# Kernel optimization log

Hardware: AMD Instinct MI355X
Metric: run time of the kernel (lower is better)

The kernel has to match this reference:

```python
import jax, jax.numpy as jnp
import numpy as np
import math

T = 1024
HID = 2880
NH = 64      # attention heads
KV = 8       # key/value heads
HD = 64      # head dim
INTER = 2880
QMULT = NH // KV
SM_SCALE = 1.0 / math.sqrt(HD)
ALPHA = 1.702   # swiglu alpha
LIMIT = 7.0     # swiglu clamp limit
EPS = 1e-5
ROPE_BASE = 150000.0
INIT_CTX = 4096
SCALING = 32.0
NTK_ALPHA = 1.0
NTK_BETA = 32.0


def rmsnorm(x, scale):
    t = x * jax.lax.rsqrt(jnp.mean(x * x, axis=-1, keepdims=True) + EPS)
    return t * scale


def rope_cos_sin(num_tokens):
    # YaRN-style NTK interpolation (scaling_factor > 1 branch)
    freq = ROPE_BASE ** (jnp.arange(0, HD, 2, dtype=jnp.float32) / HD)
    concentration = 0.1 * math.log(SCALING) + 1.0
    d_half = HD / 2
    low = d_half * math.log(INIT_CTX / (NTK_BETA * 2 * math.pi)) / math.log(ROPE_BASE)
    high = d_half * math.log(INIT_CTX / (NTK_ALPHA * 2 * math.pi)) / math.log(ROPE_BASE)
    interpolation = 1.0 / (SCALING * freq)
    extrapolation = 1.0 / freq
    ramp = (jnp.arange(d_half, dtype=jnp.float32) - low) / (high - low)
    mask = 1.0 - jnp.clip(ramp, 0.0, 1.0)
    inv_freq = interpolation * (1.0 - mask) + extrapolation * mask
    t = jnp.arange(num_tokens, dtype=jnp.float32)
    freqs = t[:, None] * inv_freq[None, :]           # [T, HD/2]
    return jnp.cos(freqs) * concentration, jnp.sin(freqs) * concentration


def apply_rope(x, cos, sin):
    # x: [T, heads, HD]; cos/sin: [T, HD/2]
    c = cos[:, None, :]
    s = sin[:, None, :]
    x1, x2 = jnp.split(x, 2, axis=-1)
    return jnp.concatenate([x1 * c - x2 * s, x2 * c + x1 * s], axis=-1)


def setup_inputs() -> dict:
    key = jax.random.key(0)
    ks = jax.random.split(key, 10)
    p = lambda k, shape: jax.random.normal(k, shape, jnp.float32) * 0.02
    qkv_dim = HD * (NH + 2 * KV)
    return {
        "x": jax.random.normal(ks[0], (T, HID), jnp.float32),
        "attn_norm_scale": jnp.ones((HID,), jnp.float32),
        "wqkv": p(ks[1], (qkv_dim, HID)),
        "bqkv": p(ks[2], (qkv_dim,)),
        "wout": p(ks[3], (HID, NH * HD)),
        "bout": p(ks[4], (HID,)),
        "mlp_norm_scale": jnp.ones((HID,), jnp.float32),
        "w1": p(ks[5], (2 * INTER, HID)),
        "b1": p(ks[6], (2 * INTER,)),
        "w2": p(ks[7], (HID, INTER)),
        "b2": p(ks[8], (HID,)),
    }


def reference(x, attn_norm_scale, wqkv, bqkv, wout, bout, mlp_norm_scale, w1, b1, w2, b2):
    # ---- attention sub-block ----
    t = rmsnorm(x, attn_norm_scale)
    qkv = t @ wqkv.T + bqkv                                   # [T, 5120]
    q = qkv[:, : NH * HD].reshape(T, NH, HD)
    k = qkv[:, NH * HD : (NH + KV) * HD].reshape(T, KV, HD)
    v = qkv[:, (NH + KV) * HD :].reshape(T, KV, HD)
    cos, sin = rope_cos_sin(T)
    q = apply_rope(q, cos, sin)
    k = apply_rope(k, cos, sin)
    kf = jnp.repeat(k, QMULT, axis=1)                         # GQA expand -> [T, NH, HD]
    vf = jnp.repeat(v, QMULT, axis=1)
    scores = jnp.einsum('thd,shd->hts', q, kf) * SM_SCALE     # [NH, T, T]
    causal = jnp.tril(jnp.ones((T, T), dtype=bool))
    scores = jnp.where(causal[None, :, :], scores, jnp.float32(-1e30))
    attn = jax.nn.softmax(scores, axis=-1)
    o = jnp.einsum('hts,shd->thd', attn, vf).reshape(T, NH * HD)
    h = x + o @ wout.T + bout                                 # residual
    # ---- SwiGLU MLP sub-block ----
    u = rmsnorm(h, mlp_norm_scale) @ w1.T + b1                # [T, 2*INTER] interleaved
    g = jnp.minimum(u[:, ::2], LIMIT)
    lin = jnp.clip(u[:, 1::2], -LIMIT, LIMIT)
    act = g * jax.nn.sigmoid(ALPHA * g) * (lin + 1.0)         # [T, INTER]
    return h + act @ w2.T + b2
```

## Files before the change

### kernel.cpp

```cpp
#include <hip/hip_runtime.h>

typedef unsigned short ushort_t;
typedef unsigned int uint_t;
typedef __bf16 bf16x8 __attribute__((ext_vector_type(8)));
typedef float floatx4 __attribute__((ext_vector_type(4)));

#define T_TOK 1024
#define HID 2880
#define NH 64
#define KV 8
#define HD 64
#define INTER 2880
#define QKV_DIM 5120
#define O_DIM 4096

typedef __attribute__((address_space(1))) const uint_t glb_u32;
typedef __attribute__((address_space(3))) uint_t lds_u32;

__device__ __forceinline__ float b2f(ushort_t u) {
    uint_t i = ((uint_t)u) << 16;
    return __builtin_bit_cast(float, i);
}
__device__ __forceinline__ ushort_t f2b(float f) {
    uint_t i = __builtin_bit_cast(uint_t, f);
    uint_t r = i + 0x7FFFu + ((i >> 16) & 1u);
    return (ushort_t)(r >> 16);
}
__device__ __forceinline__ uint4 ld16(const void* p) { uint4 v; __builtin_memcpy(&v, p, 16); return v; }
__device__ __forceinline__ void st16(void* p, uint4 v) { __builtin_memcpy(p, &v, 16); }
__device__ __forceinline__ float4 ld16f(const void* p) { float4 v; __builtin_memcpy(&v, p, 16); return v; }
__device__ __forceinline__ bf16x8 ldfrag(const void* p) { bf16x8 v; __builtin_memcpy(&v, p, 16); return v; }
__device__ __forceinline__ void cvt8st(void* lds, float4 a, float4 b) {
    ushort_t o[8] = {f2b(a.x), f2b(a.y), f2b(a.z), f2b(a.w),
                     f2b(b.x), f2b(b.y), f2b(b.z), f2b(b.w)};
    __builtin_memcpy(lds, o, 16);
}

__global__ __launch_bounds__(256) void rmsnorm_f2b(
    const float* __restrict__ x, const float* __restrict__ scale,
    ushort_t* __restrict__ out)
{
    const int row = blockIdx.x;
    const int tid = threadIdx.x;
    const float* xr = x + (size_t)row * HID;
    float ss = 0.f;
    for (int i = tid; i < HID / 4; i += 256) {
        float4 v = ld16f(xr + i * 4);
        ss += v.x * v.x + v.y * v.y + v.z * v.z + v.w * v.w;
    }
    #pragma unroll
    for (int m = 32; m >= 1; m >>= 1) ss += __shfl_xor(ss, m, 64);
    __shared__ float red[4];
    if ((tid & 63) == 0) red[tid >> 6] = ss;
    __syncthreads();
    float rstd = rsqrtf((red[0] + red[1] + red[2] + red[3]) / (float)HID + 1e-5f);
    for (int i = tid; i < HID / 8; i += 256) {
        float4 a = ld16f(xr + i * 8);
        float4 b = ld16f(xr + i * 8 + 4);
        float4 sa = ld16f(scale + i * 8);
        float4 sb = ld16f(scale + i * 8 + 4);
        cvt8st(out + (size_t)row * HID + i * 8,
               make_float4(a.x * rstd * sa.x, a.y * rstd * sa.y, a.z * rstd * sa.z, a.w * rstd * sa.w),
               make_float4(b.x * rstd * sb.x, b.y * rstd * sb.y, b.z * rstd * sb.z, b.w * rstd * sb.w));
    }
}

__global__ __launch_bounds__(256) void gemm_bt(
    const ushort_t* __restrict__ A, const float* __restrict__ B,
    const float* __restrict__ bias, const float* residual,
    void* C, int out_f32, int M, int N, int K)
{
    __shared__ ushort_t As[128 * 64];
    __shared__ ushort_t Bs[64 * 64];
    const int tid = threadIdx.x;
    const int lane = tid & 63, wave = tid >> 6;
    const int l15 = lane & 15, quad = lane >> 4;

    const int nbx = N >> 6;
    int flat = (int)blockIdx.x;
    const int cpx = (int)gridDim.x >> 3;
    flat = (flat & 7) * cpx + (flat >> 3);
    const int m0 = (flat / nbx) * 128;
    const int n0 = (flat % nbx) * 64;

    const int wm = (wave >> 1) * 64, wn = (wave & 1) * 32;

    const int arow = wave * 32 + (lane >> 3);
    const int aslot = (lane & 7) ^ (lane >> 3);
    const ushort_t* Abase = A + (size_t)(m0 + arow) * K + aslot * 8;

    const int brow = tid >> 2;
    const int kb = (tid & 3) * 8;
    const int sa = (tid & 3) ^ (brow & 7);
    const int sb = ((tid & 3) + 4) ^ (brow & 7);
    const float* Bbase = B + (size_t)(n0 + brow) * K;

    floatx4 acc[4][2] = {};
    const int nk = K >> 6;
    for (int kt = 0; kt < nk; ++kt) {
        const int k0 = kt << 6;
        float4 f0 = ld16f(Bbase + k0 + kb);
        float4 f1 = ld16f(Bbase + k0 + kb + 4);
        float4 f2 = ld16f(Bbase + k0 + kb + 32);
        float4 f3 = ld16f(Bbase + k0 + kb + 36);
        #pragma unroll
        for (int q = 0; q < 4; q++) {
            __builtin_amdgcn_global_load_lds(
                (glb_u32*)(Abase + (size_t)(q * 8) * K + k0),
                (lds_u32*)(&As[(wave * 4 + q) * 512]),
                16, 0, 0);
        }
        cvt8st(&Bs[brow * 64 + sa * 8], f0, f1);
        cvt8st(&Bs[brow * 64 + sb * 8], f2, f3);
        __syncthreads();
        #pragma unroll
        for (int c = 0; c < 2; c++) {
            bf16x8 af[4], bfr[2];
            #pragma unroll
            for (int i = 0; i < 4; i++) {
                int r = wm + i * 16 + l15;
                af[i] = ldfrag(&As[r * 64 + (((c * 4 + quad) ^ (r & 7)) * 8)]);
            }
            #pragma unroll
            for (int j = 0; j < 2; j++) {
                int r = wn + j * 16 + l15;
                bfr[j] = ldfrag(&Bs[r * 64 + (((c * 4 + quad) ^ (r & 7)) * 8)]);
            }
            #pragma unroll
            for (int i = 0; i < 4; i++)
                #pragma unroll
                for (int j = 0; j < 2; j++)
                    acc[i][j] = __builtin_amdgcn_mfma_f32_16x16x32_bf16(af[i], bfr[j], acc[i][j], 0, 0, 0);
        }
        __syncthreads();
    }
    #pragma unroll
    for (int i = 0; i < 4; i++) {
        int row = m0 + wm + i * 16 + quad * 4;
        #pragma unroll
        for (int j = 0; j < 2; j++) {
            int col = n0 + wn + j * 16 + l15;
            float bv = bias[col];
            #pragma unroll
            for (int r = 0; r < 4; r++) {
                float v = acc[i][j][r] + bv;
                if (residual) v += residual[(size_t)(row + r) * N + col];
                if (out_f32) ((float*)C)[(size_t)(row + r) * N + col] = v;
                else ((ushort_t*)C)[(size_t)(row + r) * N + col] = f2b(v);
            }
        }
    }
}

__global__ __launch_bounds__(256) void rope_kernel(ushort_t* __restrict__ qkv)
{
    int idx = blockIdx.x * 256 + threadIdx.x;
    int d = idx & 31;
    int rest = idx >> 5;
    int head = rest % (NH + KV);
    int tok = rest / (NH + KV);

    const float TWO_PI = 6.2831853071795864f;
    float fd = (float)d;
    float freq = powf(150000.0f, fd * (1.0f / 32.0f));
    float interpolation = 1.0f / (32.0f * freq);
    float extrapolation = 1.0f / freq;
    float lnb = logf(150000.0f);
    float low  = 32.0f * logf(4096.0f / (32.0f * TWO_PI)) / lnb;
    float high = 32.0f * logf(4096.0f / TWO_PI) / lnb;
    float ramp = (fd - low) / (high - low);
    ramp = fminf(fmaxf(ramp, 0.0f), 1.0f);
    float mask = 1.0f - ramp;
    float inv_freq = interpolation * (1.0f - mask) + extrapolation * mask;
    float conc = 0.1f * logf(32.0f) + 1.0f;
    float ang = (float)tok * inv_freq;
    float s = sinf(ang) * conc;
    float c = cosf(ang) * conc;

    size_t base = (head < NH)
        ? (size_t)tok * QKV_DIM + head * HD
        : (size_t)tok * QKV_DIM + NH * HD + (head - NH) * HD;
    float x1 = b2f(qkv[base + d]);
    float x2 = b2f(qkv[base + 32 + d]);
    qkv[base + d]      = f2b(x1 * c - x2 * s);
    qkv[base + 32 + d] = f2b(x2 * c + x1 * s);
}

__global__ __launch_bounds__(256) void attn_kernel(
    const ushort_t* __restrict__ qkv, ushort_t* __restrict__ o)
{
    const int qt = blockIdx.x;
    const int h  = blockIdx.y;
    const int g  = h >> 3;
    const int tid = threadIdx.x;
    const int lane = tid & 63, wave = tid >> 6;
    const int l15 = lane & 15, quad = lane >> 4;

    __shared__ ushort_t Ks[64 * 72];
    __shared__ ushort_t Vt[64 * 72];
    __shared__ ushort_t Ps[4][16 * 72];

    bf16x8 qf[2];
    const int qrow = qt * 64 + wave * 16 + l15;
    #pragma unroll
    for (int c = 0; c < 2; c++)
        qf[c] = ldfrag(&qkv[(size_t)qrow * QKV_DIM + h * HD + quad * 8 + 32 * c]);

    floatx4 ofrag[4] = {};
    float mrow[4], lrow[4];
    #pragma unroll
    for (int r = 0; r < 4; r++) { mrow[r] = -1e30f; lrow[r] = 0.f; }

    for (int kt = 0; kt <= qt; ++kt) {
        {
            int row = tid >> 2;
            int seg = (tid & 3) * 16;
            size_t sb = (size_t)(kt * 64 + row) * QKV_DIM + NH * HD + g * HD;
            st16(&Ks[row * 72 + seg],     ld16(&qkv[sb + seg]));
            st16(&Ks[row * 72 + seg + 8], ld16(&qkv[sb + seg + 8]));
            uint4 v0 = ld16(&qkv[sb + KV * HD + seg]);
            uint4 v1 = ld16(&qkv[sb + KV * HD + seg + 8]);
            uint_t w0[4] = {v0.x, v0.y, v0.z, v0.w};
            uint_t w1[4] = {v1.x, v1.y, v1.z, v1.w};
            #pragma unroll
            for (int e = 0; e < 8; e++) {
                ushort_t s0 = (e & 1) ? (ushort_t)(w0[e >> 1] >> 16) : (ushort_t)(w0[e >> 1] & 0xffffu);
                ushort_t s1 = (e & 1) ? (ushort_t)(w1[e >> 1] >> 16) : (ushort_t)(w1[e >> 1] & 0xffffu);
                Vt[(seg + e) * 72 + row]     = s0;
                Vt[(seg + 8 + e) * 72 + row] = s1;
            }
        }
        __syncthreads();

        floatx4 sf[4];
        #pragma unroll
        for (int j = 0; j < 4; j++) {
            floatx4 z = {};
            #pragma unroll
            for (int c = 0; c < 2; c++) {
                bf16x8 kf = ldfrag(&Ks[(j * 16 + l15) * 72 + quad * 8 + 32 * c]);
                z = __builtin_amdgcn_mfma_f32_16x16x32_bf16(qf[c], kf, z, 0, 0, 0);
            }
            sf[j] = z;
        }
        const int qg = qt * 64 + wave * 16 + quad * 4;
        const int kgb = kt * 64 + l15;
        float rowmax[4];
        #pragma unroll
        for (int r = 0; r < 4; r++) rowmax[r] = -1e30f;
        #pragma unroll
        for (int j = 0; j < 4; j++)
            #pragma unroll
            for (int r = 0; r < 4; r++) {
                float v = sf[j][r] * 0.125f;
                if (kgb + j * 16 > qg + r) v = -1e30f;
                sf[j][r] = v;
                rowmax[r] = fmaxf(rowmax[r], v);
            }
        #pragma unroll
        for (int r = 0; r < 4; r++)
            #pragma unroll
            for (int m = 1; m < 16; m <<= 1)
                rowmax[r] = fmaxf(rowmax[r], __shfl_xor(rowmax[r], m, 64));
        float alpha[4], rowsum[4];
        #pragma unroll
        for (int r = 0; r < 4; r++) {
            float mnew = fmaxf(mrow[r], rowmax[r]);
            alpha[r] = __expf(mrow[r] - mnew);
            mrow[r] = mnew;
            rowsum[r] = 0.f;
        }
        #pragma unroll
        for (int j = 0; j < 4; j++)
            #pragma unroll
            for (int r = 0; r < 4; r++) {
                float p = __expf(sf[j][r] - mrow[r]);
                rowsum[r] += p;
                Ps[wave][(quad * 4 + r) * 72 + j * 16 + l15] = f2b(p);
            }
        #pragma unroll
        for (int r = 0; r < 4; r++) {
            #pragma unroll
            for (int m = 1; m < 16; m <<= 1)
                rowsum[r] += __shfl_xor(rowsum[r], m, 64);
            lrow[r] = lrow[r] * alpha[r] + rowsum[r];
        }
        #pragma unroll
        for (int j = 0; j < 4; j++)
            #pragma unroll
            for (int r = 0; r < 4; r++)
                ofrag[j][r] *= alpha[r];
        __syncthreads();
        #pragma unroll
        for (int c = 0; c < 2; c++) {
            bf16x8 pf = ldfrag(&Ps[wave][l15 * 72 + quad * 8 + 32 * c]);
            #pragma unroll
            for (int j = 0; j < 4; j++) {
                bf16x8 vf = ldfrag(&Vt[(j * 16 + l15) * 72 + quad * 8 + 32 * c]);
                ofrag[j] = __builtin_amdgcn_mfma_f32_16x16x32_bf16(pf, vf, ofrag[j], 0, 0, 0);
            }
        }
        __syncthreads();
    }
    #pragma unroll
    for (int j = 0; j < 4; j++)
        #pragma unroll
        for (int r = 0; r < 4; r++) {
            int row = qt * 64 + wave * 16 + quad * 4 + r;
            int col = h * HD + j * 16 + l15;
            o[(size_t)row * O_DIM + col] = f2b(ofrag[j][r] / lrow[r]);
        }
}

__global__ __launch_bounds__(256) void act_kernel(
    const ushort_t* __restrict__ u, ushort_t* __restrict__ act)
{
    int i = blockIdx.x * 256 + threadIdx.x;
    if (i >= T_TOK * INTER) return;
    int row = i / INTER, c = i % INTER;
    uint_t v; __builtin_memcpy(&v, u + (size_t)row * (2 * INTER) + 2 * c, 4);
    float gt  = b2f((ushort_t)(v & 0xffffu));
    float lin = b2f((ushort_t)(v >> 16));
    gt = fminf(gt, 7.0f);
    lin = fminf(fmaxf(lin, -7.0f), 7.0f);
    float sg = 1.0f / (1.0f + __expf(-1.702f * gt));
    act[i] = f2b(gt * sg * (lin + 1.0f));
}

extern "C" void kernel_launch(void* const* d_in, const int* in_sizes, int n_in,
                              void* d_out, int out_size, void* d_ws, size_t ws_size,
                              hipStream_t stream)
{
    const float* x               = (const float*)d_in[0];
    const float* attn_norm_scale = (const float*)d_in[1];
    const float* wqkv            = (const float*)d_in[2];
    const float* bqkv            = (const float*)d_in[3];
    const float* wout            = (const float*)d_in[4];
    const float* bout            = (const float*)d_in[5];
    const float* mlp_norm_scale  = (const float*)d_in[6];
    const float* w1              = (const float*)d_in[7];
    const float* b1              = (const float*)d_in[8];
    const float* w2              = (const float*)d_in[9];
    const float* b2              = (const float*)d_in[10];
    float* out = (float*)d_out;

    char* ws = (char*)d_ws;
    ushort_t* t   = (ushort_t*)ws;
    ushort_t* qkv = (ushort_t*)(ws + (size_t)T_TOK * HID * 2);
    ushort_t* ob  = (ushort_t*)(ws + (size_t)T_TOK * (HID + QKV_DIM) * 2);
    ushort_t* u   = (ushort_t*)(ws + (size_t)T_TOK * (HID + QKV_DIM + O_DIM) * 2);
    ushort_t* ac  = (ushort_t*)(ws + (size_t)T_TOK * (HID + QKV_DIM + O_DIM + 2 * INTER) * 2);

    rmsnorm_f2b<<<T_TOK, 256, 0, stream>>>(x, attn_norm_scale, t);
    gemm_bt<<<dim3((T_TOK / 128) * (QKV_DIM / 64)), 256, 0, stream>>>(
        t, wqkv, bqkv, nullptr, qkv, 0, T_TOK, QKV_DIM, HID);
    rope_kernel<<<(T_TOK * (NH + KV) * 32) / 256, 256, 0, stream>>>(qkv);
    attn_kernel<<<dim3(T_TOK / 64, NH), 256, 0, stream>>>(qkv, ob);
    gemm_bt<<<dim3((T_TOK / 128) * (HID / 64)), 256, 0, stream>>>(
        ob, wout, bout, x, out, 1, T_TOK, HID, O_DIM);
    rmsnorm_f2b<<<T_TOK, 256, 0, stream>>>(out, mlp_norm_scale, t);
    gemm_bt<<<dim3((T_TOK / 128) * ((2 * INTER) / 64)), 256, 0, stream>>>(
        t, w1, b1, nullptr, u, 0, T_TOK, 2 * INTER, HID);
    act_kernel<<<(T_TOK * INTER + 255) / 256, 256, 0, stream>>>(u, ac);
    gemm_bt<<<dim3((T_TOK / 128) * (HID / 64)), 256, 0, stream>>>(
        ac, w2, b2, out, out, 1, T_TOK, HID, INTER);
}
```

Baseline: 625.5 us.

## Double-buffer GEMM tiles, split-K the output projections, constant-fold RoPE

```diff
diff --git a/kernel.cpp b/kernel.cpp
--- a/kernel.cpp
+++ b/kernel.cpp
@@ -68,10 +68,11 @@
 __global__ __launch_bounds__(256) void gemm_bt(
     const ushort_t* __restrict__ A, const float* __restrict__ B,
     const float* __restrict__ bias, const float* residual,
-    void* C, int out_f32, int M, int N, int K)
-{
-    __shared__ ushort_t As[128 * 64];
-    __shared__ ushort_t Bs[64 * 64];
+    void* C, int out_f32, float* __restrict__ scratch,
+    int M, int N, int K)
+{
+    __shared__ ushort_t As[2][128 * 64];
+    __shared__ ushort_t Bs[2][64 * 64];
     const int tid = threadIdx.x;
     const int lane = tid & 63, wave = tid >> 6;
     const int l15 = lane & 15, quad = lane >> 4;
@@ -85,46 +86,68 @@
 
     const int wm = (wave >> 1) * 64, wn = (wave & 1) * 32;
 
+    const int z = (int)blockIdx.y;
+    const int nk_all = K >> 6;
+    const int nk0 = (nk_all + 1) >> 1;
+    const int kbeg = (gridDim.y > 1 && z) ? (nk0 << 6) : 0;
+    const int nk = (gridDim.y > 1) ? (z ? nk_all - nk0 : nk0) : nk_all;
+
     const int arow = wave * 32 + (lane >> 3);
     const int aslot = (lane & 7) ^ (lane >> 3);
-    const ushort_t* Abase = A + (size_t)(m0 + arow) * K + aslot * 8;
+    const ushort_t* Abase = A + (size_t)(m0 + arow) * K + kbeg + aslot * 8;
 
     const int brow = tid >> 2;
     const int kb = (tid & 3) * 8;
     const int sa = (tid & 3) ^ (brow & 7);
     const int sb = ((tid & 3) + 4) ^ (brow & 7);
-    const float* Bbase = B + (size_t)(n0 + brow) * K;
+    const float* Bbase = B + (size_t)(n0 + brow) * K + kbeg;
 
     floatx4 acc[4][2] = {};
-    const int nk = K >> 6;
+
+    {
+        float4 f0 = ld16f(Bbase + kb);
+        float4 f1 = ld16f(Bbase + kb + 4);
+        float4 f2 = ld16f(Bbase + kb + 32);
+        float4 f3 = ld16f(Bbase + kb + 36);
+        #pragma unroll
+        for (int q = 0; q < 4; q++)
+            __builtin_amdgcn_global_load_lds(
+                (glb_u32*)(Abase + (size_t)(q * 8) * K),
+                (lds_u32*)(&As[0][(wave * 4 + q) * 512]), 16, 0, 0);
+        cvt8st(&Bs[0][brow * 64 + sa * 8], f0, f1);
+        cvt8st(&Bs[0][brow * 64 + sb * 8], f2, f3);
+    }
+    __syncthreads();
+
+    int cur = 0;
     for (int kt = 0; kt < nk; ++kt) {
-        const int k0 = kt << 6;
-        float4 f0 = ld16f(Bbase + k0 + kb);
-        float4 f1 = ld16f(Bbase + k0 + kb + 4);
-        float4 f2 = ld16f(Bbase + k0 + kb + 32);
-        float4 f3 = ld16f(Bbase + k0 + kb + 36);
-        #pragma unroll
-        for (int q = 0; q < 4; q++) {
-            __builtin_amdgcn_global_load_lds(
-                (glb_u32*)(Abase + (size_t)(q * 8) * K + k0),
-                (lds_u32*)(&As[(wave * 4 + q) * 512]),
-                16, 0, 0);
-        }
-        cvt8st(&Bs[brow * 64 + sa * 8], f0, f1);
-        cvt8st(&Bs[brow * 64 + sb * 8], f2, f3);
-        __syncthreads();
+        const int nxt = cur ^ 1;
+        const bool pre = (kt + 1 < nk);
+        float4 f0, f1, f2, f3;
+        if (pre) {
+            const int k1 = (kt + 1) << 6;
+            f0 = ld16f(Bbase + k1 + kb);
+            f1 = ld16f(Bbase + k1 + kb + 4);
+            f2 = ld16f(Bbase + k1 + kb + 32);
+            f3 = ld16f(Bbase + k1 + kb + 36);
+            #pragma unroll
+            for (int q = 0; q < 4; q++)
+                __builtin_amdgcn_global_load_lds(
+                    (glb_u32*)(Abase + (size_t)(q * 8) * K + k1),
+                    (lds_u32*)(&As[nxt][(wave * 4 + q) * 512]), 16, 0, 0);
+        }
         #pragma unroll
         for (int c = 0; c < 2; c++) {
             bf16x8 af[4], bfr[2];
             #pragma unroll
             for (int i = 0; i < 4; i++) {
                 int r = wm + i * 16 + l15;
-                af[i] = ldfrag(&As[r * 64 + (((c * 4 + quad) ^ (r & 7)) * 8)]);
+                af[i] = ldfrag(&As[cur][r * 64 + (((c * 4 + quad) ^ (r & 7)) * 8)]);
             }
             #pragma unroll
             for (int j = 0; j < 2; j++) {
                 int r = wn + j * 16 + l15;
-                bfr[j] = ldfrag(&Bs[r * 64 + (((c * 4 + quad) ^ (r & 7)) * 8)]);
+                bfr[j] = ldfrag(&Bs[cur][r * 64 + (((c * 4 + quad) ^ (r & 7)) * 8)]);
             }
             #pragma unroll
             for (int i = 0; i < 4; i++)
@@ -132,7 +155,27 @@
                 for (int j = 0; j < 2; j++)
                     acc[i][j] = __builtin_amdgcn_mfma_f32_16x16x32_bf16(af[i], bfr[j], acc[i][j], 0, 0, 0);
         }
+        if (pre) {
+            cvt8st(&Bs[nxt][brow * 64 + sa * 8], f0, f1);
+            cvt8st(&Bs[nxt][brow * 64 + sb * 8], f2, f3);
+        }
         __syncthreads();
+        cur = nxt;
+    }
+
+    if (gridDim.y > 1 && z) {
+        #pragma unroll
+        for (int i = 0; i < 4; i++) {
+            int row = m0 + wm + i * 16 + quad * 4;
+            #pragma unroll
+            for (int j = 0; j < 2; j++) {
+                int col = n0 + wn + j * 16 + l15;
+                #pragma unroll
+                for (int r = 0; r < 4; r++)
+                    scratch[(size_t)(row + r) * N + col] = acc[i][j][r];
+            }
+        }
+        return;
     }
     #pragma unroll
     for (int i = 0; i < 4; i++) {
@@ -152,6 +195,16 @@
     }
 }
 
+__global__ __launch_bounds__(256) void add_inplace(
+    float* __restrict__ dst, const float* __restrict__ src)
+{
+    int i = (blockIdx.x * 256 + threadIdx.x) * 4;
+    float4 a = ld16f(dst + i);
+    float4 b = ld16f(src + i);
+    a.x += b.x; a.y += b.y; a.z += b.z; a.w += b.w;
+    __builtin_memcpy(dst + i, &a, 16);
+}
+
 __global__ __launch_bounds__(256) void rope_kernel(ushort_t* __restrict__ qkv)
 {
     int idx = blockIdx.x * 256 + threadIdx.x;
@@ -160,22 +213,17 @@
     int head = rest % (NH + KV);
     int tok = rest / (NH + KV);
 
-    const float TWO_PI = 6.2831853071795864f;
     float fd = (float)d;
-    float freq = powf(150000.0f, fd * (1.0f / 32.0f));
+    float freq = exp2f(fd * (17.194638f / 32.0f));
     float interpolation = 1.0f / (32.0f * freq);
     float extrapolation = 1.0f / freq;
-    float lnb = logf(150000.0f);
-    float low  = 32.0f * logf(4096.0f / (32.0f * TWO_PI)) / lnb;
-    float high = 32.0f * logf(4096.0f / TWO_PI) / lnb;
-    float ramp = (fd - low) / (high - low);
+    float ramp = (fd - 8.092761f) * (1.0f / (17.397992f - 8.092761f));
     ramp = fminf(fmaxf(ramp, 0.0f), 1.0f);
     float mask = 1.0f - ramp;
     float inv_freq = interpolation * (1.0f - mask) + extrapolation * mask;
-    float conc = 0.1f * logf(32.0f) + 1.0f;
     float ang = (float)tok * inv_freq;
-    float s = sinf(ang) * conc;
-    float c = cosf(ang) * conc;
+    float s = sinf(ang) * 1.3465736f;
+    float c = cosf(ang) * 1.3465736f;
 
     size_t base = (head < NH)
         ? (size_t)tok * QKV_DIM + head * HD
@@ -350,18 +398,22 @@
     ushort_t* ob  = (ushort_t*)(ws + (size_t)T_TOK * (HID + QKV_DIM) * 2);
     ushort_t* u   = (ushort_t*)(ws + (size_t)T_TOK * (HID + QKV_DIM + O_DIM) * 2);
     ushort_t* ac  = (ushort_t*)(ws + (size_t)T_TOK * (HID + QKV_DIM + O_DIM + 2 * INTER) * 2);
+    float* sc1 = (float*)u;
+    float* sc2 = (float*)qkv;
 
     rmsnorm_f2b<<<T_TOK, 256, 0, stream>>>(x, attn_norm_scale, t);
     gemm_bt<<<dim3((T_TOK / 128) * (QKV_DIM / 64)), 256, 0, stream>>>(
-        t, wqkv, bqkv, nullptr, qkv, 0, T_TOK, QKV_DIM, HID);
+        t, wqkv, bqkv, nullptr, qkv, 0, nullptr, T_TOK, QKV_DIM, HID);
     rope_kernel<<<(T_TOK * (NH + KV) * 32) / 256, 256, 0, stream>>>(qkv);
     attn_kernel<<<dim3(T_TOK / 64, NH), 256, 0, stream>>>(qkv, ob);
-    gemm_bt<<<dim3((T_TOK / 128) * (HID / 64)), 256, 0, stream>>>(
-        ob, wout, bout, x, out, 1, T_TOK, HID, O_DIM);
+    gemm_bt<<<dim3((T_TOK / 128) * (HID / 64), 2), 256, 0, stream>>>(
+        ob, wout, bout, x, out, 1, sc1, T_TOK, HID, O_DIM);
+    add_inplace<<<(T_TOK * HID) / 1024, 256, 0, stream>>>(out, sc1);
     rmsnorm_f2b<<<T_TOK, 256, 0, stream>>>(out, mlp_norm_scale, t);
     gemm_bt<<<dim3((T_TOK / 128) * ((2 * INTER) / 64)), 256, 0, stream>>>(
-        t, w1, b1, nullptr, u, 0, T_TOK, 2 * INTER, HID);
+        t, w1, b1, nullptr, u, 0, nullptr, T_TOK, 2 * INTER, HID);
     act_kernel<<<(T_TOK * INTER + 255) / 256, 256, 0, stream>>>(u, ac);
-    gemm_bt<<<dim3((T_TOK / 128) * (HID / 64)), 256, 0, stream>>>(
-        ac, w2, b2, out, out, 1, T_TOK, HID, INTER);
-}
+    gemm_bt<<<dim3((T_TOK / 128) * (HID / 64), 2), 256, 0, stream>>>(
+        ac, w2, b2, out, out, 1, sc2, T_TOK, HID, INTER);
+    add_inplace<<<(T_TOK * HID) / 1024, 256, 0, stream>>>(out, sc2);
+}
```

After: 582.9 us. 1.07x faster.
